# Kernel optimization log

Hardware: AMD Instinct MI355X
Metric: run time of the kernel (lower is better)

The kernel has to match this reference:

```python
import jax, jax.numpy as jnp
import numpy as np

B, N, C = 1, 6400, 256
NUM_CAMS, NUM_HEADS, NUM_LEVELS, NUM_POINTS = 6, 8, 3, 8
LVL_SHAPES = [(64, 176), (32, 88), (16, 44)]
IMG_H, IMG_W = 512, 1408


def setup_inputs():
    key = jax.random.key(0)
    ks = jax.random.split(key, 16)
    # Gaussian means in ego frame: depth z in [2,40]; x/y scaled so projections land in-image
    z = jax.random.uniform(ks[0], (B, N, 1), minval=2.0, maxval=40.0)
    xy = jax.random.uniform(ks[1], (B, N, 2), minval=-0.5, maxval=0.5)
    means = jnp.concatenate([xy[..., 0:1] * z * 0.8, xy[..., 1:2] * z * 0.4, z], -1)
    feature = jax.random.normal(ks[2], (B, N, C)) * 0.5
    feat0 = jax.random.normal(ks[3], (B * NUM_CAMS, C, 64, 176)) * 0.5
    feat1 = jax.random.normal(ks[4], (B * NUM_CAMS, C, 32, 88)) * 0.5
    feat2 = jax.random.normal(ks[5], (B * NUM_CAMS, C, 16, 44)) * 0.5
    cam2ego = jnp.tile(jnp.eye(4), (B, NUM_CAMS, 1, 1))
    cam2ego = cam2ego.at[..., :3, 3].set(jax.random.uniform(ks[6], (B, NUM_CAMS, 3), minval=-0.5, maxval=0.5))
    intrins = jnp.tile(jnp.array([[500., 0., 704.], [0., 500., 256.], [0., 0., 1.]]), (B, NUM_CAMS, 1, 1))
    post_rots = jnp.tile(jnp.eye(3), (B, NUM_CAMS, 1, 1))
    post_trans = jnp.concatenate([jax.random.uniform(ks[7], (B, NUM_CAMS, 2), minval=-30., maxval=30.),
                                  jnp.zeros((B, NUM_CAMS, 1))], -1)
    # deformable-attn style bias init for sampling offsets (as in init_weights)
    thetas = np.arange(NUM_HEADS) * (2.0 * np.pi / NUM_HEADS)
    grid = np.stack([np.cos(thetas), np.sin(thetas)], -1)
    grid = grid / np.abs(grid).max(-1, keepdims=True)
    grid = np.tile(grid.reshape(NUM_HEADS, 1, 1, 2), (1, NUM_LEVELS, NUM_POINTS, 1))
    grid = grid * (np.arange(NUM_POINTS) + 1).reshape(1, 1, NUM_POINTS, 1)
    b_off = jnp.asarray(grid.reshape(-1), jnp.float32)
    W_off = jax.random.normal(ks[8], (C, NUM_HEADS * NUM_LEVELS * NUM_POINTS * 2)) * 0.01
    W_attn = jax.random.normal(ks[9], (C, NUM_HEADS * NUM_LEVELS * NUM_POINTS)) * 0.02
    b_attn = jnp.zeros((NUM_HEADS * NUM_LEVELS * NUM_POINTS,))
    W_val = jax.random.normal(ks[10], (C, C)) * (1.0 / np.sqrt(C))
    b_val = jnp.zeros((C,))
    W_out = jax.random.normal(ks[11], (C, C)) * (1.0 / np.sqrt(C))
    b_out = jnp.zeros((C,))
    cams_embeds = jax.random.normal(ks[12], (NUM_CAMS, C))
    level_embeds = jax.random.normal(ks[13], (NUM_LEVELS, C))
    ln_g = jnp.ones((C,))
    ln_b = jnp.zeros((C,))
    return dict(means=means, feature=feature, feat0=feat0, feat1=feat1, feat2=feat2,
                cam2ego=cam2ego, intrins=intrins, post_rots=post_rots, post_trans=post_trans,
                W_off=W_off, b_off=b_off, W_attn=W_attn, b_attn=b_attn, W_val=W_val, b_val=b_val,
                W_out=W_out, b_out=b_out, cams_embeds=cams_embeds, level_embeds=level_embeds,
                ln_g=ln_g, ln_b=ln_b, img_h=IMG_H, img_w=IMG_W)


def _msda(value, shapes, loc, attn):
    # Multi-scale deformable attention (matches multi_scale_deformable_attn_pytorch,
    # i.e. grid_sample bilinear, align_corners=False, zero padding).
    # value [Bc,S,H,D]; loc [Bc,Nq,H,L,P,2] in [0,1]; attn [Bc,Nq,H,L,P]
    Bc, S, Hh, D = value.shape
    Nq, P = loc.shape[1], loc.shape[4]
    out = jnp.zeros((Bc, Hh, Nq, D), value.dtype)
    start = 0
    for lvl, (h, w) in enumerate(shapes):
        v = value[:, start:start + h * w].transpose(0, 2, 1, 3)  # [Bc,H,h*w,D]
        l = loc[:, :, :, lvl]                                    # [Bc,Nq,H,P,2]
        x = l[..., 0] * w - 0.5  # align_corners=False pixel coords
        y = l[..., 1] * h - 0.5
        x0 = jnp.floor(x)
        y0 = jnp.floor(y)
        tx = x - x0
        ty = y - y0
        a = attn[:, :, :, lvl]                                   # [Bc,Nq,H,P]
        def samp(xi, yi, wgt):
            valid = (xi >= 0) & (xi <= w - 1) & (yi >= 0) & (yi <= h - 1)
            idx = (jnp.clip(yi, 0, h - 1) * w + jnp.clip(xi, 0, w - 1)).astype(jnp.int32)
            idx = idx.transpose(0, 2, 1, 3).reshape(Bc, Hh, Nq * P)
            g = jnp.take_along_axis(v, idx[..., None], axis=2)   # [Bc,H,Nq*P,D]
            coef = wgt * jnp.where(valid, 1.0, 0.0).astype(v.dtype) * a
            return g * coef.transpose(0, 2, 1, 3).reshape(Bc, Hh, Nq * P, 1)
        acc = (samp(x0, y0, (1 - tx) * (1 - ty)) + samp(x0 + 1, y0, tx * (1 - ty))
               + samp(x0, y0 + 1, (1 - tx) * ty) + samp(x0 + 1, y0 + 1, tx * ty))
        out = out + acc.reshape(Bc, Hh, Nq, P, D).sum(3)
        start += h * w
    return out.transpose(0, 2, 1, 3).reshape(Bc, Nq, Hh * D)


def reference(means, feature, feat0, feat1, feat2, cam2ego, intrins, post_rots, post_trans,
              W_off, b_off, W_attn, b_attn, W_val, b_val, W_out, b_out,
              cams_embeds, level_embeds, ln_g, ln_b, img_h, img_w):
    Bq, Nq, Cc = feature.shape
    D = Cc // NUM_HEADS
    # --- project reference points into each camera (project_reference_points) ---
    mh = jnp.concatenate([means, jnp.ones((Bq, Nq, 1), means.dtype)], -1)      # [B,N,4]
    means_cam = jnp.einsum('bcij,bnj->bcni', jnp.linalg.inv(cam2ego), mh)[..., :3]
    means_img = jnp.einsum('bcij,bcnj->bcni', intrins, means_cam)              # [B,cams,N,3]
    mi = jnp.concatenate([means_img[..., :2] / (means_img[..., 2:] + 1e-4), means_img[..., 2:]], -1)
    mi = jnp.einsum('bcij,bcnj->bcni', post_rots, mi) + post_trans[:, :, None, :]
    coor = mi[..., :2] / jnp.array([img_w, img_h], feature.dtype)              # [B,cams,N,2]
    depth = mi[..., 2]
    mask = ((depth > 0.01) & (coor[..., 0] > 0.) & (coor[..., 0] < 1.)
            & (coor[..., 1] > 0.) & (coor[..., 1] < 1.))                        # [B,cams,N]
    # --- per-query sampling offsets / attention weights (shared across cameras) ---
    offsets = (feature @ W_off + b_off).reshape(Bq, Nq, NUM_HEADS, NUM_LEVELS, NUM_POINTS, 2)
    attn = jax.nn.softmax((feature @ W_attn + b_attn).reshape(Bq, Nq, NUM_HEADS, NUM_LEVELS * NUM_POINTS), -1)
    attn = attn.reshape(Bq, Nq, NUM_HEADS, NUM_LEVELS, NUM_POINTS)
    # --- flatten multi-level feats + cam/level embeds, value projection ---
    feats = (feat0, feat1, feat2)
    shapes = [(f.shape[2], f.shape[3]) for f in feats]
    flat = []
    for lvl, f in enumerate(feats):
        h, w = shapes[lvl]
        fl = f.reshape(Bq, NUM_CAMS, Cc, h * w)
        fl = fl + cams_embeds[None, :, :, None] + level_embeds[lvl][None, None, :, None]
        flat.append(fl)
    value = jnp.concatenate(flat, -1).transpose(0, 1, 3, 2).reshape(Bq * NUM_CAMS, -1, Cc)
    value = (value @ W_val + b_val).reshape(Bq * NUM_CAMS, -1, NUM_HEADS, D)
    # --- sampling locations per camera ---
    norm = jnp.array([[w, h] for (h, w) in shapes], feature.dtype)             # [L,2] = (W_l,H_l)
    loc = coor[:, :, :, None, None, None, :] + offsets[:, None] / norm[None, None, None, None, :, None, :]
    loc = loc.reshape(Bq * NUM_CAMS, Nq, NUM_HEADS, NUM_LEVELS, NUM_POINTS, 2)
    attn_bc = jnp.broadcast_to(attn[:, None], (Bq, NUM_CAMS, Nq, NUM_HEADS, NUM_LEVELS, NUM_POINTS))
    attn_bc = attn_bc.reshape(Bq * NUM_CAMS, Nq, NUM_HEADS, NUM_LEVELS, NUM_POINTS)
    out = _msda(value, shapes, loc, attn_bc).reshape(Bq, NUM_CAMS, Nq, Cc)
    # --- mask-weighted combine over cameras (mathematically equals the rebatch/scatter) ---
    mf = mask.astype(feature.dtype)
    slots = (out * mf[..., None]).sum(1) / jnp.maximum(mf.sum(1), 1.0)[..., None]
    slots = slots @ W_out + b_out
    x = slots + feature  # dropout is identity at inference
    mu = jnp.mean(x, -1, keepdims=True)
    var = jnp.mean((x - mu) ** 2, -1, keepdims=True)
    return (x - mu) / jnp.sqrt(var + 1e-5) * ln_g + ln_b
```

## Files before the change

### kernel.cpp

```cpp
#include <hip/hip_runtime.h>
#include <hip/hip_bf16.h>

typedef __bf16 bf16;
typedef __attribute__((ext_vector_type(4))) float f32x4;
typedef __attribute__((ext_vector_type(8))) bf16 bf16x8;
typedef __attribute__((ext_vector_type(2))) bf16 bf16x2;

#define NCAMS 6
#define NQ 6400
#define CH 256
#define NH 8
#define NL 3
#define NP 8
#define S_TOT 14784

#if __has_builtin(__builtin_amdgcn_fdot2_f32_bf16) && __has_builtin(__builtin_amdgcn_perm)
#define MSDA_DOT2 1
#else
#define MSDA_DOT2 0
#endif

__global__ __launch_bounds__(256) void k_prep(
    const float* __restrict__ means, const float* __restrict__ cam2ego,
    const float* __restrict__ intrins, const float* __restrict__ post_rots,
    const float* __restrict__ post_trans, const int* __restrict__ img_h,
    const int* __restrict__ img_w,
    const float* __restrict__ W_val, const float* __restrict__ W_off,
    const float* __restrict__ W_attn, const float* __restrict__ W_out,
    float* __restrict__ coor, float* __restrict__ maskf,
    bf16* __restrict__ Wvp, bf16* __restrict__ Woap, bf16* __restrict__ Wop)
{
    int bid = blockIdx.x;
    if (bid < 150) {
        int idx = bid * 256 + threadIdx.x;
        if (idx >= NCAMS * NQ) return;
        int cam = idx / NQ, n = idx % NQ;
        float mx = means[n*3+0], my = means[n*3+1], mz = means[n*3+2];
        const float* M = cam2ego + cam*16;
        float R[3][3], t[3];
        #pragma unroll
        for (int r = 0; r < 3; r++) {
            #pragma unroll
            for (int c = 0; c < 3; c++) R[r][c] = M[r*4+c];
            t[r] = M[r*4+3];
        }
        float dx = mx - t[0], dy = my - t[1], dz = mz - t[2];
        float xc = R[0][0]*dx + R[1][0]*dy + R[2][0]*dz;
        float yc = R[0][1]*dx + R[1][1]*dy + R[2][1]*dz;
        float zc = R[0][2]*dx + R[1][2]*dy + R[2][2]*dz;
        const float* K = intrins + cam*9;
        float ix = K[0]*xc + K[1]*yc + K[2]*zc;
        float iy = K[3]*xc + K[4]*yc + K[5]*zc;
        float iz = K[6]*xc + K[7]*yc + K[8]*zc;
        float px = ix / (iz + 1e-4f), py = iy / (iz + 1e-4f), pz = iz;
        const float* P = post_rots + cam*9;
        const float* T = post_trans + cam*3;
        float vx = P[0]*px + P[1]*py + P[2]*pz + T[0];
        float vy = P[3]*px + P[4]*py + P[5]*pz + T[1];
        float vz = P[6]*px + P[7]*py + P[8]*pz + T[2];
        float cx = vx / (float)img_w[0];
        float cy = vy / (float)img_h[0];
        bool ok = (vz > 0.01f) && (cx > 0.f) && (cx < 1.f) && (cy > 0.f) && (cy < 1.f);
        coor[idx*2+0] = cx;
        coor[idx*2+1] = cy;
        maskf[idx] = ok ? 1.f : 0.f;
        return;
    }
    int flat = (bid - 150) * 256 + threadIdx.x;
    if (flat < 8192) {
        int kc = flat >> 10, rem = flat & 1023;
        int nf = rem >> 6, lane = rem & 63;
        int q = lane >> 4, col = nf*16 + (lane & 15);
        bf16x8 v;
        #pragma unroll
        for (int j = 0; j < 8; j++) v[j] = (bf16)W_val[(size_t)(kc*32 + q*8 + j)*256 + col];
        *reinterpret_cast<bf16x8*>(Wvp + (size_t)flat*8) = v;
    } else if (flat < 26624) {
        int f2 = flat - 8192;
        int kc = f2 / (36*64), rem = f2 % (36*64);
        int nf = rem >> 6, lane = rem & 63;
        int q = lane >> 4, col = nf*16 + (lane & 15);
        bf16x8 v;
        #pragma unroll
        for (int j = 0; j < 8; j++) {
            int k = kc*32 + q*8 + j;
            float x = (col < 384) ? W_off[(size_t)k*384 + col] : W_attn[(size_t)k*192 + (col-384)];
            v[j] = (bf16)x;
        }
        *reinterpret_cast<bf16x8*>(Woap + (size_t)f2*8) = v;
    } else if (flat < 34816) {
        int f3 = flat - 26624;
        int kc = f3 >> 10, rem = f3 & 1023;
        int nf = rem >> 6, lane = rem & 63;
        int q = lane >> 4, col = nf*16 + (lane & 15);
        bf16x8 v;
        #pragma unroll
        for (int j = 0; j < 8; j++) v[j] = (bf16)W_out[(size_t)(kc*32 + q*8 + j)*256 + col];
        *reinterpret_cast<bf16x8*>(Wop + (size_t)f3*8) = v;
    }
}

__global__ __launch_bounds__(256) void k_offattn2(
    const float* __restrict__ feature, const bf16* __restrict__ Woap,
    const float* __restrict__ b_off, const float* __restrict__ b_attn,
    float* __restrict__ offs, bf16* __restrict__ attn_out)
{
    __shared__ float lg[16][200];
    int t = threadIdx.x, lane = t & 63, w = t >> 6;
    int q = lane >> 4, r16 = lane & 15;
    int n0 = blockIdx.x * 16;

    f32x4 acc[9];
    #pragma unroll
    for (int i = 0; i < 9; i++) acc[i] = (f32x4){0.f,0.f,0.f,0.f};

    const float* arow = feature + (size_t)(n0 + r16)*CH;
    for (int kc = 0; kc < 8; kc++) {
        f32x4 a0 = *reinterpret_cast<const f32x4*>(arow + kc*32 + q*8);
        f32x4 a1 = *reinterpret_cast<const f32x4*>(arow + kc*32 + q*8 + 4);
        bf16x8 afr;
        #pragma unroll
        for (int i = 0; i < 4; i++) { afr[i] = (bf16)a0[i]; afr[4+i] = (bf16)a1[i]; }
        #pragma unroll
        for (int nf9 = 0; nf9 < 9; nf9++) {
            bf16x8 bfr = *reinterpret_cast<const bf16x8*>(Woap + ((size_t)(kc*36 + w*9 + nf9)*64 + lane)*8);
            acc[nf9] = __builtin_amdgcn_mfma_f32_16x16x32_bf16(afr, bfr, acc[nf9], 0, 0, 0);
        }
    }
    #pragma unroll
    for (int nf9 = 0; nf9 < 9; nf9++) {
        int nfg = w*9 + nf9;
        int nglob = nfg*16 + r16;
        if (nfg < 24) {
            float bias = b_off[nglob];
            #pragma unroll
            for (int r = 0; r < 4; r++)
                offs[(size_t)(n0 + q*4 + r)*384 + nglob] = acc[nf9][r] + bias;
        } else {
            int la = nglob - 384;
            float bias = b_attn[la];
            #pragma unroll
            for (int r = 0; r < 4; r++)
                lg[q*4 + r][la] = acc[nf9][r] + bias;
        }
    }
    __syncthreads();
    if (t < 128) {
        int m = t >> 3, h = t & 7;
        const float* L = &lg[m][h*24];
        float mx = -1e30f;
        #pragma unroll
        for (int j = 0; j < 24; j++) mx = fmaxf(mx, L[j]);
        float e[24]; float s = 0.f;
        #pragma unroll
        for (int j = 0; j < 24; j++) { e[j] = __expf(L[j] - mx); s += e[j]; }
        float inv = 1.f / s;
        #pragma unroll
        for (int j = 0; j < 24; j++) attn_out[(size_t)(n0+m)*192 + h*24 + j] = (bf16)(e[j]*inv);
    }
}

__global__ __launch_bounds__(256) void k_valproj(
    const float* __restrict__ f0, const float* __restrict__ f1, const float* __restrict__ f2,
    const float* __restrict__ cams_embeds, const float* __restrict__ level_embeds,
    const bf16* __restrict__ Wvp, const float* __restrict__ b_val, bf16* __restrict__ value)
{
    __shared__ alignas(16) bf16 A[64][48];
    __shared__ alignas(16) bf16 Cst[16][256];
    int bi = blockIdx.x;
    int cam = bi / 231, mb = bi % 231;
    int lvl, local0, HW;
    const float* fp;
    if (mb < 176)      { lvl = 0; local0 = mb*64;        fp = f0; HW = 11264; }
    else if (mb < 220) { lvl = 1; local0 = (mb-176)*64;  fp = f1; HW = 2816;  }
    else               { lvl = 2; local0 = (mb-220)*64;  fp = f2; HW = 704;   }
    int pos0 = (lvl == 0 ? 0 : (lvl == 1 ? 11264 : 14080)) + local0;
    const float* featbase = fp + (size_t)cam*CH*HW + local0;

    int t = threadIdx.x;
    int lane = t & 63, w = t >> 6;
    int kk = t >> 3;
    int m8 = (t & 7) * 8;
    int q = lane >> 4, r16 = lane & 15;

    f32x4 acc[4][4];
    #pragma unroll
    for (int i = 0; i < 4; i++)
        #pragma unroll
        for (int j = 0; j < 4; j++) acc[i][j] = (f32x4){0.f,0.f,0.f,0.f};

    for (int kc = 0; kc < 8; kc++) {
        __syncthreads();
        int kg = kc*32 + kk;
        float e = cams_embeds[cam*CH + kg] + level_embeds[lvl*CH + kg];
        f32x4 v0 = *reinterpret_cast<const f32x4*>(featbase + (size_t)kg*HW + m8);
        f32x4 v1 = *reinterpret_cast<const f32x4*>(featbase + (size_t)kg*HW + m8 + 4);
        #pragma unroll
        for (int i = 0; i < 4; i++) A[m8+i][kk]   = (bf16)(v0[i] + e);
        #pragma unroll
        for (int i = 0; i < 4; i++) A[m8+4+i][kk] = (bf16)(v1[i] + e);
        __syncthreads();

        bf16x8 bfr[4];
        #pragma unroll
        for (int nf = 0; nf < 4; nf++) {
            int nfg = w*4 + nf;
            bfr[nf] = *reinterpret_cast<const bf16x8*>(Wvp + ((size_t)(kc*16 + nfg)*64 + lane)*8);
        }
        #pragma unroll
        for (int mf = 0; mf < 4; mf++) {
            bf16x8 afr = *reinterpret_cast<const bf16x8*>(&A[mf*16 + r16][q*8]);
            #pragma unroll
            for (int nf = 0; nf < 4; nf++)
                acc[mf][nf] = __builtin_amdgcn_mfma_f32_16x16x32_bf16(afr, bfr[nf], acc[mf][nf], 0, 0, 0);
        }
    }
    int orow = t >> 4;
    int ocol = (t & 15) * 16;
    int ohead = ocol >> 5, och = ocol & 31;
    #pragma unroll
    for (int mf = 0; mf < 4; mf++) {
        __syncthreads();
        #pragma unroll
        for (int nf = 0; nf < 4; nf++) {
            int c = w*64 + nf*16 + r16;
            float bv = b_val[c];
            #pragma unroll
            for (int r = 0; r < 4; r++)
                Cst[q*4 + r][c] = (bf16)(acc[mf][nf][r] + bv);
        }
        __syncthreads();
        int srow = pos0 + mf*16 + orow;
        bf16* dst = value + ((size_t)(cam*NH + ohead)*S_TOT + srow)*32 + och;
        const f32x4* src = reinterpret_cast<const f32x4*>(&Cst[orow][ocol]);
        f32x4 x0 = src[0], x1 = src[1];
        reinterpret_cast<f32x4*>(dst)[0] = x0;
        reinterpret_cast<f32x4*>(dst)[1] = x1;
    }
}

__global__ __launch_bounds__(256) void k_msda(
    const float* __restrict__ coor, const float* __restrict__ offs,
    const bf16* __restrict__ attn, const bf16* __restrict__ value,
    const float* __restrict__ maskf, float* __restrict__ slots)
{
    __shared__ int4  s_o[NCAMS*192];
#if MSDA_DOT2
    __shared__ uint2 s_w[NCAMS*192];
#else
    __shared__ f32x4 s_w[NCAMS*192];
#endif
    int n = blockIdx.x;
    int t = threadIdx.x;

    for (int it = t; it < NCAMS*192; it += 256) {
        int cam = it / 192;
        int r   = it - cam*192;
        int hh  = r / 24;
        int rr  = r - hh*24;
        int lvl = rr >> 3;

        float mk = maskf[cam*NQ + n];
        float cx = coor[(cam*NQ + n)*2 + 0];
        float cy = coor[(cam*NQ + n)*2 + 1];
        float2 o2 = *reinterpret_cast<const float2*>(offs + (size_t)n*384 + r*2);
        float aw = (float)attn[(size_t)n*192 + r] * mk;

        int wi   = (lvl == 0) ? 176 : ((lvl == 1) ? 88 : 44);
        int hi   = (lvl == 0) ? 64  : ((lvl == 1) ? 32 : 16);
        int base = (lvl == 0) ? 0   : ((lvl == 1) ? 11264 : 14080);

        float x = cx*(float)wi + o2.x - 0.5f;
        float y = cy*(float)hi + o2.y - 0.5f;
        float xf = floorf(x), yf = floorf(y);
        float tx = x - xf, ty = y - yf;
        float wm1x = (float)(wi-1), wm1y = (float)(hi-1);
        bool vx0 = (xf >= 0.f)      && (xf <= wm1x);
        bool vx1 = (xf+1.f >= 0.f)  && (xf+1.f <= wm1x);
        bool vy0 = (yf >= 0.f)      && (yf <= wm1y);
        bool vy1 = (yf+1.f >= 0.f)  && (yf+1.f <= wm1y);
        int x0 = (int)fminf(fmaxf(xf,      0.f), wm1x);
        int x1 = (int)fminf(fmaxf(xf+1.f,  0.f), wm1x);
        int y0 = (int)fminf(fmaxf(yf,      0.f), wm1y);
        int y1 = (int)fminf(fmaxf(yf+1.f,  0.f), wm1y);
        float w00 = (1.f-tx)*(1.f-ty)*aw * ((vx0 && vy0) ? 1.f : 0.f);
        float w10 = tx*(1.f-ty)*aw       * ((vx1 && vy0) ? 1.f : 0.f);
        float w01 = (1.f-tx)*ty*aw       * ((vx0 && vy1) ? 1.f : 0.f);
        float w11 = tx*ty*aw             * ((vx1 && vy1) ? 1.f : 0.f);
        int rowb = (cam*NH + hh)*S_TOT + base;
        int r0 = rowb + y0*wi, r1 = rowb + y1*wi;
        s_o[it] = make_int4((r0 + x0)*64, (r0 + x1)*64, (r1 + x0)*64, (r1 + x1)*64);
#if MSDA_DOT2
        bf16x2 wa; wa[0] = (bf16)w00; wa[1] = (bf16)w10;
        bf16x2 wb; wb[0] = (bf16)w01; wb[1] = (bf16)w11;
        s_w[it] = make_uint2(__builtin_bit_cast(unsigned, wa),
                             __builtin_bit_cast(unsigned, wb));
#else
        s_w[it] = (f32x4){w00, w10, w01, w11};
#endif
    }
    __syncthreads();

    int lane = t & 63, wv = t >> 6;
    int hl = lane >> 5;
    int p  = (lane >> 2) & 7;
    int k2 = lane & 3;
    int hglob = wv*2 + hl;
    int kb = k2 * 16;
    int ibase = hglob*24 + p;

    f32x4 acc0 = (f32x4){0.f,0.f,0.f,0.f};
    f32x4 acc1 = (f32x4){0.f,0.f,0.f,0.f};
    const char* vbyte = (const char*)value;

    #pragma unroll 2
    for (int cam = 0; cam < NCAMS; cam++) {
        #pragma unroll
        for (int lvl = 0; lvl < 3; lvl++) {
            int it = cam*192 + ibase + lvl*8;
            int4  o4 = s_o[it];
#if MSDA_DOT2
            uint2 wp = s_w[it];
            bf16x2 wa = __builtin_bit_cast(bf16x2, wp.x);
            bf16x2 wb = __builtin_bit_cast(bf16x2, wp.y);
            uint4 d00 = *reinterpret_cast<const uint4*>(vbyte + (o4.x + kb));
            uint4 d10 = *reinterpret_cast<const uint4*>(vbyte + (o4.y + kb));
            uint4 d01 = *reinterpret_cast<const uint4*>(vbyte + (o4.z + kb));
            uint4 d11 = *reinterpret_cast<const uint4*>(vbyte + (o4.w + kb));
            unsigned a0 = __builtin_amdgcn_perm(d10.x, d00.x, 0x05040100u);
            unsigned a1 = __builtin_amdgcn_perm(d10.x, d00.x, 0x07060302u);
            unsigned a2 = __builtin_amdgcn_perm(d10.y, d00.y, 0x05040100u);
            unsigned a3 = __builtin_amdgcn_perm(d10.y, d00.y, 0x07060302u);
            unsigned a4 = __builtin_amdgcn_perm(d10.z, d00.z, 0x05040100u);
            unsigned a5 = __builtin_amdgcn_perm(d10.z, d00.z, 0x07060302u);
            unsigned a6 = __builtin_amdgcn_perm(d10.w, d00.w, 0x05040100u);
            unsigned a7 = __builtin_amdgcn_perm(d10.w, d00.w, 0x07060302u);
            acc0[0] = __builtin_amdgcn_fdot2_f32_bf16(__builtin_bit_cast(bf16x2, a0), wa, acc0[0], false);
            acc0[1] = __builtin_amdgcn_fdot2_f32_bf16(__builtin_bit_cast(bf16x2, a1), wa, acc0[1], false);
            acc0[2] = __builtin_amdgcn_fdot2_f32_bf16(__builtin_bit_cast(bf16x2, a2), wa, acc0[2], false);
            acc0[3] = __builtin_amdgcn_fdot2_f32_bf16(__builtin_bit_cast(bf16x2, a3), wa, acc0[3], false);
            acc1[0] = __builtin_amdgcn_fdot2_f32_bf16(__builtin_bit_cast(bf16x2, a4), wa, acc1[0], false);
            acc1[1] = __builtin_amdgcn_fdot2_f32_bf16(__builtin_bit_cast(bf16x2, a5), wa, acc1[1], false);
            acc1[2] = __builtin_amdgcn_fdot2_f32_bf16(__builtin_bit_cast(bf16x2, a6), wa, acc1[2], false);
            acc1[3] = __builtin_amdgcn_fdot2_f32_bf16(__builtin_bit_cast(bf16x2, a7), wa, acc1[3], false);
            unsigned b0 = __builtin_amdgcn_perm(d11.x, d01.x, 0x05040100u);
            unsigned b1 = __builtin_amdgcn_perm(d11.x, d01.x, 0x07060302u);
            unsigned b2 = __builtin_amdgcn_perm(d11.y, d01.y, 0x05040100u);
            unsigned b3 = __builtin_amdgcn_perm(d11.y, d01.y, 0x07060302u);
            unsigned b4 = __builtin_amdgcn_perm(d11.z, d01.z, 0x05040100u);
            unsigned b5 = __builtin_amdgcn_perm(d11.z, d01.z, 0x07060302u);
            unsigned b6 = __builtin_amdgcn_perm(d11.w, d01.w, 0x05040100u);
            unsigned b7 = __builtin_amdgcn_perm(d11.w, d01.w, 0x07060302u);
            acc0[0] = __builtin_amdgcn_fdot2_f32_bf16(__builtin_bit_cast(bf16x2, b0), wb, acc0[0], false);
            acc0[1] = __builtin_amdgcn_fdot2_f32_bf16(__builtin_bit_cast(bf16x2, b1), wb, acc0[1], false);
            acc0[2] = __builtin_amdgcn_fdot2_f32_bf16(__builtin_bit_cast(bf16x2, b2), wb, acc0[2], false);
            acc0[3] = __builtin_amdgcn_fdot2_f32_bf16(__builtin_bit_cast(bf16x2, b3), wb, acc0[3], false);
            acc1[0] = __builtin_amdgcn_fdot2_f32_bf16(__builtin_bit_cast(bf16x2, b4), wb, acc1[0], false);
            acc1[1] = __builtin_amdgcn_fdot2_f32_bf16(__builtin_bit_cast(bf16x2, b5), wb, acc1[1], false);
            acc1[2] = __builtin_amdgcn_fdot2_f32_bf16(__builtin_bit_cast(bf16x2, b6), wb, acc1[2], false);
            acc1[3] = __builtin_amdgcn_fdot2_f32_bf16(__builtin_bit_cast(bf16x2, b7), wb, acc1[3], false);
#else
            f32x4 w4 = s_w[it];
            uint4 d00 = *reinterpret_cast<const uint4*>(vbyte + (o4.x + kb));
            uint4 d10 = *reinterpret_cast<const uint4*>(vbyte + (o4.y + kb));
            uint4 d01 = *reinterpret_cast<const uint4*>(vbyte + (o4.z + kb));
            uint4 d11 = *reinterpret_cast<const uint4*>(vbyte + (o4.w + kb));
            acc0[0] = fmaf(__uint_as_float(d00.x << 16),         w4.x, acc0[0]);
            acc0[1] = fmaf(__uint_as_float(d00.x & 0xffff0000u), w4.x, acc0[1]);
            acc0[2] = fmaf(__uint_as_float(d00.y << 16),         w4.x, acc0[2]);
            acc0[3] = fmaf(__uint_as_float(d00.y & 0xffff0000u), w4.x, acc0[3]);
            acc1[0] = fmaf(__uint_as_float(d00.z << 16),         w4.x, acc1[0]);
            acc1[1] = fmaf(__uint_as_float(d00.z & 0xffff0000u), w4.x, acc1[1]);
            acc1[2] = fmaf(__uint_as_float(d00.w << 16),         w4.x, acc1[2]);
            acc1[3] = fmaf(__uint_as_float(d00.w & 0xffff0000u), w4.x, acc1[3]);
            acc0[0] = fmaf(__uint_as_float(d10.x << 16),         w4.y, acc0[0]);
            acc0[1] = fmaf(__uint_as_float(d10.x & 0xffff0000u), w4.y, acc0[1]);
            acc0[2] = fmaf(__uint_as_float(d10.y << 16),         w4.y, acc0[2]);
            acc0[3] = fmaf(__uint_as_float(d10.y & 0xffff0000u), w4.y, acc0[3]);
            acc1[0] = fmaf(__uint_as_float(d10.z << 16),         w4.y, acc1[0]);
            acc1[1] = fmaf(__uint_as_float(d10.z & 0xffff0000u), w4.y, acc1[1]);
            acc1[2] = fmaf(__uint_as_float(d10.w << 16),         w4.y, acc1[2]);
            acc1[3] = fmaf(__uint_as_float(d10.w & 0xffff0000u), w4.y, acc1[3]);
            acc0[0] = fmaf(__uint_as_float(d01.x << 16),         w4.z, acc0[0]);
            acc0[1] = fmaf(__uint_as_float(d01.x & 0xffff0000u), w4.z, acc0[1]);
            acc0[2] = fmaf(__uint_as_float(d01.y << 16),         w4.z, acc0[2]);
            acc0[3] = fmaf(__uint_as_float(d01.y & 0xffff0000u), w4.z, acc0[3]);
            acc1[0] = fmaf(__uint_as_float(d01.z << 16),         w4.z, acc1[0]);
            acc1[1] = fmaf(__uint_as_float(d01.z & 0xffff0000u), w4.z, acc1[1]);
            acc1[2] = fmaf(__uint_as_float(d01.w << 16),         w4.z, acc1[2]);
            acc1[3] = fmaf(__uint_as_float(d01.w & 0xffff0000u), w4.z, acc1[3]);
            acc0[0] = fmaf(__uint_as_float(d11.x << 16),         w4.w, acc0[0]);
            acc0[1] = fmaf(__uint_as_float(d11.x & 0xffff0000u), w4.w, acc0[1]);
            acc0[2] = fmaf(__uint_as_float(d11.y << 16),         w4.w, acc0[2]);
            acc0[3] = fmaf(__uint_as_float(d11.y & 0xffff0000u), w4.w, acc0[3]);
            acc1[0] = fmaf(__uint_as_float(d11.z << 16),         w4.w, acc1[0]);
            acc1[1] = fmaf(__uint_as_float(d11.z & 0xffff0000u), w4.w, acc1[1]);
            acc1[2] = fmaf(__uint_as_float(d11.w << 16),         w4.w, acc1[2]);
            acc1[3] = fmaf(__uint_as_float(d11.w & 0xffff0000u), w4.w, acc1[3]);
#endif
        }
    }

    #pragma unroll
    for (int i = 0; i < 4; i++) {
        acc0[i] += __shfl_xor(acc0[i], 4);
        acc0[i] += __shfl_xor(acc0[i], 8);
        acc0[i] += __shfl_xor(acc0[i], 16);
        acc1[i] += __shfl_xor(acc1[i], 4);
        acc1[i] += __shfl_xor(acc1[i], 8);
        acc1[i] += __shfl_xor(acc1[i], 16);
    }
    if (p == 0) {
        float* dst = slots + (size_t)n*CH + hglob*32 + k2*8;
        *reinterpret_cast<f32x4*>(dst)     = acc0;
        *reinterpret_cast<f32x4*>(dst + 4) = acc1;
    }
}

__global__ __launch_bounds__(256) void k_final2(
    const float* __restrict__ slots, const float* __restrict__ maskf,
    const bf16* __restrict__ Wop, const float* __restrict__ b_out,
    const float* __restrict__ feature, const float* __restrict__ ln_g,
    const float* __restrict__ ln_b, float* __restrict__ out)
{
    __shared__ float yb[16][264];
    int t = threadIdx.x, lane = t & 63, w = t >> 6;
    int q = lane >> 4, r16 = lane & 15;
    int n0 = blockIdx.x * 16;

    float msum = 0.f;
    #pragma unroll
    for (int cam = 0; cam < NCAMS; cam++) msum += maskf[cam*NQ + n0 + r16];
    float inv = 1.f / fmaxf(msum, 1.f);

    f32x4 acc[4];
    #pragma unroll
    for (int i = 0; i < 4; i++) acc[i] = (f32x4){0.f,0.f,0.f,0.f};

    const float* srow = slots + (size_t)(n0 + r16)*CH;
    for (int kc = 0; kc < 8; kc++) {
        f32x4 a0 = *reinterpret_cast<const f32x4*>(srow + kc*32 + q*8);
        f32x4 a1 = *reinterpret_cast<const f32x4*>(srow + kc*32 + q*8 + 4);
        bf16x8 afr;
        #pragma unroll
        for (int i = 0; i < 4; i++) { afr[i] = (bf16)(a0[i]*inv); afr[4+i] = (bf16)(a1[i]*inv); }
        #pragma unroll
        for (int nf = 0; nf < 4; nf++) {
            bf16x8 bfr = *reinterpret_cast<const bf16x8*>(Wop + ((size_t)(kc*16 + w*4 + nf)*64 + lane)*8);
            acc[nf] = __builtin_amdgcn_mfma_f32_16x16x32_bf16(afr, bfr, acc[nf], 0, 0, 0);
        }
    }
    #pragma unroll
    for (int nf = 0; nf < 4; nf++) {
        int c = (w*4 + nf)*16 + r16;
        float bias = b_out[c];
        #pragma unroll
        for (int r = 0; r < 4; r++) {
            int m = q*4 + r;
            yb[m][c] = acc[nf][r] + bias + feature[(size_t)(n0+m)*CH + c];
        }
    }
    __syncthreads();
    int row = t >> 4, l16 = t & 15;
    int c0 = l16 * 16;
    float s = 0.f, s2 = 0.f;
    #pragma unroll
    for (int j = 0; j < 16; j++) {
        float v = yb[row][c0 + j];
        s += v; s2 += v*v;
    }
    #pragma unroll
    for (int off = 1; off < 16; off <<= 1) {
        s  += __shfl_xor(s, off);
        s2 += __shfl_xor(s2, off);
    }
    float mu = s / 256.f;
    float rsig = rsqrtf(s2 / 256.f - mu*mu + 1e-5f);
    float* orow = out + (size_t)(n0 + row)*CH + c0;
    #pragma unroll
    for (int j4 = 0; j4 < 4; j4++) {
        f32x4 o;
        #pragma unroll
        for (int i = 0; i < 4; i++) {
            int c = c0 + j4*4 + i;
            o[i] = (yb[row][c] - mu) * rsig * ln_g[c] + ln_b[c];
        }
        *reinterpret_cast<f32x4*>(orow + j4*4) = o;
    }
}

extern "C" void kernel_launch(void* const* d_in, const int* in_sizes, int n_in,
                              void* d_out, int out_size, void* d_ws, size_t ws_size,
                              hipStream_t stream)
{
    const float* means       = (const float*)d_in[0];
    const float* feature     = (const float*)d_in[1];
    const float* feat0       = (const float*)d_in[2];
    const float* feat1       = (const float*)d_in[3];
    const float* feat2       = (const float*)d_in[4];
    const float* cam2ego     = (const float*)d_in[5];
    const float* intrins     = (const float*)d_in[6];
    const float* post_rots   = (const float*)d_in[7];
    const float* post_trans  = (const float*)d_in[8];
    const float* W_off       = (const float*)d_in[9];
    const float* b_off       = (const float*)d_in[10];
    const float* W_attn      = (const float*)d_in[11];
    const float* b_attn      = (const float*)d_in[12];
    const float* W_val       = (const float*)d_in[13];
    const float* b_val       = (const float*)d_in[14];
    const float* W_out       = (const float*)d_in[15];
    const float* b_out       = (const float*)d_in[16];
    const float* cams_embeds = (const float*)d_in[17];
    const float* level_embeds= (const float*)d_in[18];
    const float* ln_g        = (const float*)d_in[19];
    const float* ln_b        = (const float*)d_in[20];
    const int*   img_h       = (const int*)d_in[21];
    const int*   img_w       = (const int*)d_in[22];

    char* ws = (char*)d_ws;
    float* coor  = (float*)(ws + 0);
    float* maskf = (float*)(ws + 307200);
    float* offs  = (float*)(ws + 460800);
    bf16*  attn  = (bf16*) (ws + 10291200);
    bf16*  Wvp   = (bf16*) (ws + 12748800);
    bf16*  Woap  = (bf16*) (ws + 12879872);
    bf16*  Wop   = (bf16*) (ws + 13174784);
    float* slots = (float*)(ws + 13305856);
    bf16*  value = (bf16*) (ws + 19859456);
    if (ws_size < 65275904u) return;

    k_prep    <<<286, 256, 0, stream>>>(means, cam2ego, intrins, post_rots, post_trans,
                                        img_h, img_w, W_val, W_off, W_attn, W_out,
                                        coor, maskf, Wvp, Woap, Wop);
    k_offattn2<<<400, 256, 0, stream>>>(feature, Woap, b_off, b_attn, offs, attn);
    k_valproj <<<1386, 256, 0, stream>>>(feat0, feat1, feat2, cams_embeds, level_embeds, Wvp, b_val, value);
    k_msda    <<<6400, 256, 0, stream>>>(coor, offs, attn, value, maskf, slots);
    k_final2  <<<400, 256, 0, stream>>>(slots, maskf, Wop, b_out, feature, ln_g, ln_b, (float*)d_out);
}
```

Before: 302.8 us.

## Merge offset/attn and value-projection kernels; software-pipeline MSDA gathers across cameras

Folds the offset/attention projection and the value projection into one launch, branching on block index, so both independent GEMMs share a single grid and one launch and drain. In the MSDA sampling loop, the 12 value gathers for the next camera are issued before the current camera's bilinear dot products are computed, hiding gather latency. The trade-offs are higher register pressure, which may lower occupancy, and shared memory sized for the larger of the two merged paths.

```diff
diff --git a/kernel.cpp b/kernel.cpp
--- a/kernel.cpp
+++ b/kernel.cpp
@@ -100,74 +100,76 @@
     }
 }
 
-__global__ __launch_bounds__(256) void k_offattn2(
+__global__ __launch_bounds__(256) void k_mid(
     const float* __restrict__ feature, const bf16* __restrict__ Woap,
     const float* __restrict__ b_off, const float* __restrict__ b_attn,
-    float* __restrict__ offs, bf16* __restrict__ attn_out)
-{
-    __shared__ float lg[16][200];
-    int t = threadIdx.x, lane = t & 63, w = t >> 6;
-    int q = lane >> 4, r16 = lane & 15;
-    int n0 = blockIdx.x * 16;
-
-    f32x4 acc[9];
-    #pragma unroll
-    for (int i = 0; i < 9; i++) acc[i] = (f32x4){0.f,0.f,0.f,0.f};
-
-    const float* arow = feature + (size_t)(n0 + r16)*CH;
-    for (int kc = 0; kc < 8; kc++) {
-        f32x4 a0 = *reinterpret_cast<const f32x4*>(arow + kc*32 + q*8);
-        f32x4 a1 = *reinterpret_cast<const f32x4*>(arow + kc*32 + q*8 + 4);
-        bf16x8 afr;
-        #pragma unroll
-        for (int i = 0; i < 4; i++) { afr[i] = (bf16)a0[i]; afr[4+i] = (bf16)a1[i]; }
-        #pragma unroll
-        for (int nf9 = 0; nf9 < 9; nf9++) {
-            bf16x8 bfr = *reinterpret_cast<const bf16x8*>(Woap + ((size_t)(kc*36 + w*9 + nf9)*64 + lane)*8);
-            acc[nf9] = __builtin_amdgcn_mfma_f32_16x16x32_bf16(afr, bfr, acc[nf9], 0, 0, 0);
-        }
-    }
-    #pragma unroll
-    for (int nf9 = 0; nf9 < 9; nf9++) {
-        int nfg = w*9 + nf9;
-        int nglob = nfg*16 + r16;
-        if (nfg < 24) {
-            float bias = b_off[nglob];
-            #pragma unroll
-            for (int r = 0; r < 4; r++)
-                offs[(size_t)(n0 + q*4 + r)*384 + nglob] = acc[nf9][r] + bias;
-        } else {
-            int la = nglob - 384;
-            float bias = b_attn[la];
-            #pragma unroll
-            for (int r = 0; r < 4; r++)
-                lg[q*4 + r][la] = acc[nf9][r] + bias;
-        }
-    }
-    __syncthreads();
-    if (t < 128) {
-        int m = t >> 3, h = t & 7;
-        const float* L = &lg[m][h*24];
-        float mx = -1e30f;
-        #pragma unroll
-        for (int j = 0; j < 24; j++) mx = fmaxf(mx, L[j]);
-        float e[24]; float s = 0.f;
-        #pragma unroll
-        for (int j = 0; j < 24; j++) { e[j] = __expf(L[j] - mx); s += e[j]; }
-        float inv = 1.f / s;
-        #pragma unroll
-        for (int j = 0; j < 24; j++) attn_out[(size_t)(n0+m)*192 + h*24 + j] = (bf16)(e[j]*inv);
-    }
-}
-
-__global__ __launch_bounds__(256) void k_valproj(
+    float* __restrict__ offs, bf16* __restrict__ attn_out,
     const float* __restrict__ f0, const float* __restrict__ f1, const float* __restrict__ f2,
     const float* __restrict__ cams_embeds, const float* __restrict__ level_embeds,
     const bf16* __restrict__ Wvp, const float* __restrict__ b_val, bf16* __restrict__ value)
 {
-    __shared__ alignas(16) bf16 A[64][48];
-    __shared__ alignas(16) bf16 Cst[16][256];
-    int bi = blockIdx.x;
+    __shared__ alignas(16) char smem[14336];
+    int t = threadIdx.x, lane = t & 63, w = t >> 6;
+    int q = lane >> 4, r16 = lane & 15;
+
+    if (blockIdx.x < 400) {
+        float (*lg)[200] = reinterpret_cast<float(*)[200]>(smem);
+        int n0 = blockIdx.x * 16;
+
+        f32x4 acc[9];
+        #pragma unroll
+        for (int i = 0; i < 9; i++) acc[i] = (f32x4){0.f,0.f,0.f,0.f};
+
+        const float* arow = feature + (size_t)(n0 + r16)*CH;
+        for (int kc = 0; kc < 8; kc++) {
+            f32x4 a0 = *reinterpret_cast<const f32x4*>(arow + kc*32 + q*8);
+            f32x4 a1 = *reinterpret_cast<const f32x4*>(arow + kc*32 + q*8 + 4);
+            bf16x8 afr;
+            #pragma unroll
+            for (int i = 0; i < 4; i++) { afr[i] = (bf16)a0[i]; afr[4+i] = (bf16)a1[i]; }
+            #pragma unroll
+            for (int nf9 = 0; nf9 < 9; nf9++) {
+                bf16x8 bfr = *reinterpret_cast<const bf16x8*>(Woap + ((size_t)(kc*36 + w*9 + nf9)*64 + lane)*8);
+                acc[nf9] = __builtin_amdgcn_mfma_f32_16x16x32_bf16(afr, bfr, acc[nf9], 0, 0, 0);
+            }
+        }
+        #pragma unroll
+        for (int nf9 = 0; nf9 < 9; nf9++) {
+            int nfg = w*9 + nf9;
+            int nglob = nfg*16 + r16;
+            if (nfg < 24) {
+                float bias = b_off[nglob];
+                #pragma unroll
+                for (int r = 0; r < 4; r++)
+                    offs[(size_t)(n0 + q*4 + r)*384 + nglob] = acc[nf9][r] + bias;
+            } else {
+                int la = nglob - 384;
+                float bias = b_attn[la];
+                #pragma unroll
+                for (int r = 0; r < 4; r++)
+                    lg[q*4 + r][la] = acc[nf9][r] + bias;
+            }
+        }
+        __syncthreads();
+        if (t < 128) {
+            int m = t >> 3, h = t & 7;
+            const float* L = &lg[m][h*24];
+            float mx = -1e30f;
+            #pragma unroll
+            for (int j = 0; j < 24; j++) mx = fmaxf(mx, L[j]);
+            float e[24]; float s = 0.f;
+            #pragma unroll
+            for (int j = 0; j < 24; j++) { e[j] = __expf(L[j] - mx); s += e[j]; }
+            float inv = 1.f / s;
+            #pragma unroll
+            for (int j = 0; j < 24; j++) attn_out[(size_t)(n0+m)*192 + h*24 + j] = (bf16)(e[j]*inv);
+        }
+        return;
+    }
+
+    bf16 (*A)[48]    = reinterpret_cast<bf16(*)[48]>(smem);
+    bf16 (*Cst)[256] = reinterpret_cast<bf16(*)[256]>(smem + 6144);
+    int bi = blockIdx.x - 400;
     int cam = bi / 231, mb = bi % 231;
     int lvl, local0, HW;
     const float* fp;
@@ -177,11 +179,8 @@
     int pos0 = (lvl == 0 ? 0 : (lvl == 1 ? 11264 : 14080)) + local0;
     const float* featbase = fp + (size_t)cam*CH*HW + local0;
 
-    int t = threadIdx.x;
-    int lane = t & 63, w = t >> 6;
     int kk = t >> 3;
     int m8 = (t & 7) * 8;
-    int q = lane >> 4, r16 = lane & 15;
 
     f32x4 acc[4][4];
     #pragma unroll
@@ -313,93 +312,127 @@
     f32x4 acc1 = (f32x4){0.f,0.f,0.f,0.f};
     const char* vbyte = (const char*)value;
 
-    #pragma unroll 2
+    uint4 cA0,cA1,cA2, cB0,cB1,cB2, cC0,cC1,cC2, cD0,cD1,cD2;
+#if MSDA_DOT2
+    uint2 cw0, cw1, cw2;
+#else
+    f32x4 cw0, cw1, cw2;
+#endif
+
+#define LOADBATCH(CAMIDX, A0,A1,A2, B0,B1,B2, C0,C1,C2, D0,D1,D2, W0,W1,W2) \
+    { int itb = (CAMIDX)*192 + ibase; \
+      int4 o0 = s_o[itb]; int4 o1 = s_o[itb+8]; int4 o2v = s_o[itb+16]; \
+      A0 = *reinterpret_cast<const uint4*>(vbyte + (o0.x + kb)); \
+      B0 = *reinterpret_cast<const uint4*>(vbyte + (o0.y + kb)); \
+      C0 = *reinterpret_cast<const uint4*>(vbyte + (o0.z + kb)); \
+      D0 = *reinterpret_cast<const uint4*>(vbyte + (o0.w + kb)); \
+      A1 = *reinterpret_cast<const uint4*>(vbyte + (o1.x + kb)); \
+      B1 = *reinterpret_cast<const uint4*>(vbyte + (o1.y + kb)); \
+      C1 = *reinterpret_cast<const uint4*>(vbyte + (o1.z + kb)); \
+      D1 = *reinterpret_cast<const uint4*>(vbyte + (o1.w + kb)); \
+      A2 = *reinterpret_cast<const uint4*>(vbyte + (o2v.x + kb)); \
+      B2 = *reinterpret_cast<const uint4*>(vbyte + (o2v.y + kb)); \
+      C2 = *reinterpret_cast<const uint4*>(vbyte + (o2v.z + kb)); \
+      D2 = *reinterpret_cast<const uint4*>(vbyte + (o2v.w + kb)); \
+      W0 = s_w[itb]; W1 = s_w[itb+8]; W2 = s_w[itb+16]; }
+
+#if MSDA_DOT2
+#define CONSUME1(d00, d10, d01, d11, WP) \
+    { bf16x2 wa = __builtin_bit_cast(bf16x2, (WP).x); \
+      bf16x2 wb = __builtin_bit_cast(bf16x2, (WP).y); \
+      unsigned a0 = __builtin_amdgcn_perm((d10).x, (d00).x, 0x05040100u); \
+      unsigned a1 = __builtin_amdgcn_perm((d10).x, (d00).x, 0x07060302u); \
+      unsigned a2 = __builtin_amdgcn_perm((d10).y, (d00).y, 0x05040100u); \
+      unsigned a3 = __builtin_amdgcn_perm((d10).y, (d00).y, 0x07060302u); \
+      unsigned a4 = __builtin_amdgcn_perm((d10).z, (d00).z, 0x05040100u); \
+      unsigned a5 = __builtin_amdgcn_perm((d10).z, (d00).z, 0x07060302u); \
+      unsigned a6 = __builtin_amdgcn_perm((d10).w, (d00).w, 0x05040100u); \
+      unsigned a7 = __builtin_amdgcn_perm((d10).w, (d00).w, 0x07060302u); \
+      acc0[0] = __builtin_amdgcn_fdot2_f32_bf16(__builtin_bit_cast(bf16x2, a0), wa, acc0[0], false); \
+      acc0[1] = __builtin_amdgcn_fdot2_f32_bf16(__builtin_bit_cast(bf16x2, a1), wa, acc0[1], false); \
+      acc0[2] = __builtin_amdgcn_fdot2_f32_bf16(__builtin_bit_cast(bf16x2, a2), wa, acc0[2], false); \
+      acc0[3] = __builtin_amdgcn_fdot2_f32_bf16(__builtin_bit_cast(bf16x2, a3), wa, acc0[3], false); \
+      acc1[0] = __builtin_amdgcn_fdot2_f32_bf16(__builtin_bit_cast(bf16x2, a4), wa, acc1[0], false); \
+      acc1[1] = __builtin_amdgcn_fdot2_f32_bf16(__builtin_bit_cast(bf16x2, a5), wa, acc1[1], false); \
+      acc1[2] = __builtin_amdgcn_fdot2_f32_bf16(__builtin_bit_cast(bf16x2, a6), wa, acc1[2], false); \
+      acc1[3] = __builtin_amdgcn_fdot2_f32_bf16(__builtin_bit_cast(bf16x2, a7), wa, acc1[3], false); \
+      unsigned b0 = __builtin_amdgcn_perm((d11).x, (d01).x, 0x05040100u); \
+      unsigned b1 = __builtin_amdgcn_perm((d11).x, (d01).x, 0x07060302u); \
+      unsigned b2 = __builtin_amdgcn_perm((d11).y, (d01).y, 0x05040100u); \
+      unsigned b3 = __builtin_amdgcn_perm((d11).y, (d01).y, 0x07060302u); \
+      unsigned b4 = __builtin_amdgcn_perm((d11).z, (d01).z, 0x05040100u); \
+      unsigned b5 = __builtin_amdgcn_perm((d11).z, (d01).z, 0x07060302u); \
+      unsigned b6 = __builtin_amdgcn_perm((d11).w, (d01).w, 0x05040100u); \
+      unsigned b7 = __builtin_amdgcn_perm((d11).w, (d01).w, 0x07060302u); \
+      acc0[0] = __builtin_amdgcn_fdot2_f32_bf16(__builtin_bit_cast(bf16x2, b0), wb, acc0[0], false); \
+      acc0[1] = __builtin_amdgcn_fdot2_f32_bf16(__builtin_bit_cast(bf16x2, b1), wb, acc0[1], false); \
+      acc0[2] = __builtin_amdgcn_fdot2_f32_bf16(__builtin_bit_cast(bf16x2, b2), wb, acc0[2], false); \
+      acc0[3] = __builtin_amdgcn_fdot2_f32_bf16(__builtin_bit_cast(bf16x2, b3), wb, acc0[3], false); \
+      acc1[0] = __builtin_amdgcn_fdot2_f32_bf16(__builtin_bit_cast(bf16x2, b4), wb, acc1[0], false); \
+      acc1[1] = __builtin_amdgcn_fdot2_f32_bf16(__builtin_bit_cast(bf16x2, b5), wb, acc1[1], false); \
+      acc1[2] = __builtin_amdgcn_fdot2_f32_bf16(__builtin_bit_cast(bf16x2, b6), wb, acc1[2], false); \
+      acc1[3] = __builtin_amdgcn_fdot2_f32_bf16(__builtin_bit_cast(bf16x2, b7), wb, acc1[3], false); }
+#else
+#define CONSUME1(d00, d10, d01, d11, WP) \
+    { f32x4 w4 = (WP); \
+      acc0[0] = fmaf(__uint_as_float((d00).x << 16),         w4.x, acc0[0]); \
+      acc0[1] = fmaf(__uint_as_float((d00).x & 0xffff0000u), w4.x, acc0[1]); \
+      acc0[2] = fmaf(__uint_as_float((d00).y << 16),         w4.x, acc0[2]); \
+      acc0[3] = fmaf(__uint_as_float((d00).y & 0xffff0000u), w4.x, acc0[3]); \
+      acc1[0] = fmaf(__uint_as_float((d00).z << 16),         w4.x, acc1[0]); \
+      acc1[1] = fmaf(__uint_as_float((d00).z & 0xffff0000u), w4.x, acc1[1]); \
+      acc1[2] = fmaf(__uint_as_float((d00).w << 16),         w4.x, acc1[2]); \
+      acc1[3] = fmaf(__uint_as_float((d00).w & 0xffff0000u), w4.x, acc1[3]); \
+      acc0[0] = fmaf(__uint_as_float((d10).x << 16),         w4.y, acc0[0]); \
+      acc0[1] = fmaf(__uint_as_float((d10).x & 0xffff0000u), w4.y, acc0[1]); \
+      acc0[2] = fmaf(__uint_as_float((d10).y << 16),         w4.y, acc0[2]); \
+      acc0[3] = fmaf(__uint_as_float((d10).y & 0xffff0000u), w4.y, acc0[3]); \
+      acc1[0] = fmaf(__uint_as_float((d10).z << 16),         w4.y, acc1[0]); \
+      acc1[1] = fmaf(__uint_as_float((d10).z & 0xffff0000u), w4.y, acc1[1]); \
+      acc1[2] = fmaf(__uint_as_float((d10).w << 16),         w4.y, acc1[2]); \
+      acc1[3] = fmaf(__uint_as_float((d10).w & 0xffff0000u), w4.y, acc1[3]); \
+      acc0[0] = fmaf(__uint_as_float((d01).x << 16),         w4.z, acc0[0]); \
+      acc0[1] = fmaf(__uint_as_float((d01).x & 0xffff0000u), w4.z, acc0[1]); \
+      acc0[2] = fmaf(__uint_as_float((d01).y << 16),         w4.z, acc0[2]); \
+      acc0[3] = fmaf(__uint_as_float((d01).y & 0xffff0000u), w4.z, acc0[3]); \
+      acc1[0] = fmaf(__uint_as_float((d01).z << 16),         w4.z, acc1[0]); \
+      acc1[1] = fmaf(__uint_as_float((d01).z & 0xffff0000u), w4.z, acc1[1]); \
+      acc1[2] = fmaf(__uint_as_float((d01).w << 16),         w4.z, acc1[2]); \
+      acc1[3] = fmaf(__uint_as_float((d01).w & 0xffff0000u), w4.z, acc1[3]); \
+      acc0[0] = fmaf(__uint_as_float((d11).x << 16),         w4.w, acc0[0]); \
+      acc0[1] = fmaf(__uint_as_float((d11).x & 0xffff0000u), w4.w, acc0[1]); \
+      acc0[2] = fmaf(__uint_as_float((d11).y << 16),         w4.w, acc0[2]); \
+      acc0[3] = fmaf(__uint_as_float((d11).y & 0xffff0000u), w4.w, acc0[3]); \
+      acc1[0] = fmaf(__uint_as_float((d11).z << 16),         w4.w, acc1[0]); \
+      acc1[1] = fmaf(__uint_as_float((d11).z & 0xffff0000u), w4.w, acc1[1]); \
+      acc1[2] = fmaf(__uint_as_float((d11).w << 16),         w4.w, acc1[2]); \
+      acc1[3] = fmaf(__uint_as_float((d11).w & 0xffff0000u), w4.w, acc1[3]); }
+#endif
+
+    LOADBATCH(0, cA0,cA1,cA2, cB0,cB1,cB2, cC0,cC1,cC2, cD0,cD1,cD2, cw0,cw1,cw2)
+
+    #pragma unroll
     for (int cam = 0; cam < NCAMS; cam++) {
-        #pragma unroll
-        for (int lvl = 0; lvl < 3; lvl++) {
-            int it = cam*192 + ibase + lvl*8;
-            int4  o4 = s_o[it];
+        uint4 nA0,nA1,nA2, nB0,nB1,nB2, nC0,nC1,nC2, nD0,nD1,nD2;
 #if MSDA_DOT2
-            uint2 wp = s_w[it];
-            bf16x2 wa = __builtin_bit_cast(bf16x2, wp.x);
-            bf16x2 wb = __builtin_bit_cast(bf16x2, wp.y);
-            uint4 d00 = *reinterpret_cast<const uint4*>(vbyte + (o4.x + kb));
-            uint4 d10 = *reinterpret_cast<const uint4*>(vbyte + (o4.y + kb));
-            uint4 d01 = *reinterpret_cast<const uint4*>(vbyte + (o4.z + kb));
-            uint4 d11 = *reinterpret_cast<const uint4*>(vbyte + (o4.w + kb));
-            unsigned a0 = __builtin_amdgcn_perm(d10.x, d00.x, 0x05040100u);
-            unsigned a1 = __builtin_amdgcn_perm(d10.x, d00.x, 0x07060302u);
-            unsigned a2 = __builtin_amdgcn_perm(d10.y, d00.y, 0x05040100u);
-            unsigned a3 = __builtin_amdgcn_perm(d10.y, d00.y, 0x07060302u);
-            unsigned a4 = __builtin_amdgcn_perm(d10.z, d00.z, 0x05040100u);
-            unsigned a5 = __builtin_amdgcn_perm(d10.z, d00.z, 0x07060302u);
-            unsigned a6 = __builtin_amdgcn_perm(d10.w, d00.w, 0x05040100u);
-            unsigned a7 = __builtin_amdgcn_perm(d10.w, d00.w, 0x07060302u);
-            acc0[0] = __builtin_amdgcn_fdot2_f32_bf16(__builtin_bit_cast(bf16x2, a0), wa, acc0[0], false);
-            acc0[1] = __builtin_amdgcn_fdot2_f32_bf16(__builtin_bit_cast(bf16x2, a1), wa, acc0[1], false);
-            acc0[2] = __builtin_amdgcn_fdot2_f32_bf16(__builtin_bit_cast(bf16x2, a2), wa, acc0[2], false);
-            acc0[3] = __builtin_amdgcn_fdot2_f32_bf16(__builtin_bit_cast(bf16x2, a3), wa, acc0[3], false);
-            acc1[0] = __builtin_amdgcn_fdot2_f32_bf16(__builtin_bit_cast(bf16x2, a4), wa, acc1[0], false);
-            acc1[1] = __builtin_amdgcn_fdot2_f32_bf16(__builtin_bit_cast(bf16x2, a5), wa, acc1[1], false);
-            acc1[2] = __builtin_amdgcn_fdot2_f32_bf16(__builtin_bit_cast(bf16x2, a6), wa, acc1[2], false);
-            acc1[3] = __builtin_amdgcn_fdot2_f32_bf16(__builtin_bit_cast(bf16x2, a7), wa, acc1[3], false);
-            unsigned b0 = __builtin_amdgcn_perm(d11.x, d01.x, 0x05040100u);
-            unsigned b1 = __builtin_amdgcn_perm(d11.x, d01.x, 0x07060302u);
-            unsigned b2 = __builtin_amdgcn_perm(d11.y, d01.y, 0x05040100u);
-            unsigned b3 = __builtin_amdgcn_perm(d11.y, d01.y, 0x07060302u);
-            unsigned b4 = __builtin_amdgcn_perm(d11.z, d01.z, 0x05040100u);
-            unsigned b5 = __builtin_amdgcn_perm(d11.z, d01.z, 0x07060302u);
-            unsigned b6 = __builtin_amdgcn_perm(d11.w, d01.w, 0x05040100u);
-            unsigned b7 = __builtin_amdgcn_perm(d11.w, d01.w, 0x07060302u);
-            acc0[0] = __builtin_amdgcn_fdot2_f32_bf16(__builtin_bit_cast(bf16x2, b0), wb, acc0[0], false);
-            acc0[1] = __builtin_amdgcn_fdot2_f32_bf16(__builtin_bit_cast(bf16x2, b1), wb, acc0[1], false);
-            acc0[2] = __builtin_amdgcn_fdot2_f32_bf16(__builtin_bit_cast(bf16x2, b2), wb, acc0[2], false);
-            acc0[3] = __builtin_amdgcn_fdot2_f32_bf16(__builtin_bit_cast(bf16x2, b3), wb, acc0[3], false);
-            acc1[0] = __builtin_amdgcn_fdot2_f32_bf16(__builtin_bit_cast(bf16x2, b4), wb, acc1[0], false);
-            acc1[1] = __builtin_amdgcn_fdot2_f32_bf16(__builtin_bit_cast(bf16x2, b5), wb, acc1[1], false);
-            acc1[2] = __builtin_amdgcn_fdot2_f32_bf16(__builtin_bit_cast(bf16x2, b6), wb, acc1[2], false);
-            acc1[3] = __builtin_amdgcn_fdot2_f32_bf16(__builtin_bit_cast(bf16x2, b7), wb, acc1[3], false);
+        uint2 nw0, nw1, nw2;
 #else
-            f32x4 w4 = s_w[it];
-            uint4 d00 = *reinterpret_cast<const uint4*>(vbyte + (o4.x + kb));
-            uint4 d10 = *reinterpret_cast<const uint4*>(vbyte + (o4.y + kb));
-            uint4 d01 = *reinterpret_cast<const uint4*>(vbyte + (o4.z + kb));
-            uint4 d11 = *reinterpret_cast<const uint4*>(vbyte + (o4.w + kb));
-            acc0[0] = fmaf(__uint_as_float(d00.x << 16),         w4.x, acc0[0]);
-            acc0[1] = fmaf(__uint_as_float(d00.x & 0xffff0000u), w4.x, acc0[1]);
-            acc0[2] = fmaf(__uint_as_float(d00.y << 16),         w4.x, acc0[2]);
-            acc0[3] = fmaf(__uint_as_float(d00.y & 0xffff0000u), w4.x, acc0[3]);
-            acc1[0] = fmaf(__uint_as_float(d00.z << 16),         w4.x, acc1[0]);
-            acc1[1] = fmaf(__uint_as_float(d00.z & 0xffff0000u), w4.x, acc1[1]);
-            acc1[2] = fmaf(__uint_as_float(d00.w << 16),         w4.x, acc1[2]);
-            acc1[3] = fmaf(__uint_as_float(d00.w & 0xffff0000u), w4.x, acc1[3]);
-            acc0[0] = fmaf(__uint_as_float(d10.x << 16),         w4.y, acc0[0]);
-            acc0[1] = fmaf(__uint_as_float(d10.x & 0xffff0000u), w4.y, acc0[1]);
-            acc0[2] = fmaf(__uint_as_float(d10.y << 16),         w4.y, acc0[2]);
-            acc0[3] = fmaf(__uint_as_float(d10.y & 0xffff0000u), w4.y, acc0[3]);
-            acc1[0] = fmaf(__uint_as_float(d10.z << 16),         w4.y, acc1[0]);
-            acc1[1] = fmaf(__uint_as_float(d10.z & 0xffff0000u), w4.y, acc1[1]);
-            acc1[2] = fmaf(__uint_as_float(d10.w << 16),         w4.y, acc1[2]);
-            acc1[3] = fmaf(__uint_as_float(d10.w & 0xffff0000u), w4.y, acc1[3]);
-            acc0[0] = fmaf(__uint_as_float(d01.x << 16),         w4.z, acc0[0]);
-            acc0[1] = fmaf(__uint_as_float(d01.x & 0xffff0000u), w4.z, acc0[1]);
-            acc0[2] = fmaf(__uint_as_float(d01.y << 16),         w4.z, acc0[2]);
-            acc0[3] = fmaf(__uint_as_float(d01.y & 0xffff0000u), w4.z, acc0[3]);
-            acc1[0] = fmaf(__uint_as_float(d01.z << 16),         w4.z, acc1[0]);
-            acc1[1] = fmaf(__uint_as_float(d01.z & 0xffff0000u), w4.z, acc1[1]);
-            acc1[2] = fmaf(__uint_as_float(d01.w << 16),         w4.z, acc1[2]);
-            acc1[3] = fmaf(__uint_as_float(d01.w & 0xffff0000u), w4.z, acc1[3]);
-            acc0[0] = fmaf(__uint_as_float(d11.x << 16),         w4.w, acc0[0]);
-            acc0[1] = fmaf(__uint_as_float(d11.x & 0xffff0000u), w4.w, acc0[1]);
-            acc0[2] = fmaf(__uint_as_float(d11.y << 16),         w4.w, acc0[2]);
-            acc0[3] = fmaf(__uint_as_float(d11.y & 0xffff0000u), w4.w, acc0[3]);
-            acc1[0] = fmaf(__uint_as_float(d11.z << 16),         w4.w, acc1[0]);
-            acc1[1] = fmaf(__uint_as_float(d11.z & 0xffff0000u), w4.w, acc1[1]);
-            acc1[2] = fmaf(__uint_as_float(d11.w << 16),         w4.w, acc1[2]);
-            acc1[3] = fmaf(__uint_as_float(d11.w & 0xffff0000u), w4.w, acc1[3]);
+        f32x4 nw0, nw1, nw2;
 #endif
-        }
-    }
+        if (cam + 1 < NCAMS) {
+            LOADBATCH(cam+1, nA0,nA1,nA2, nB0,nB1,nB2, nC0,nC1,nC2, nD0,nD1,nD2, nw0,nw1,nw2)
+        }
+        CONSUME1(cA0, cB0, cC0, cD0, cw0)
+        CONSUME1(cA1, cB1, cC1, cD1, cw1)
+        CONSUME1(cA2, cB2, cC2, cD2, cw2)
+        if (cam + 1 < NCAMS) {
+            cA0=nA0; cA1=nA1; cA2=nA2; cB0=nB0; cB1=nB1; cB2=nB2;
+            cC0=nC0; cC1=nC1; cC2=nC2; cD0=nD0; cD1=nD1; cD2=nD2;
+            cw0=nw0; cw1=nw1; cw2=nw2;
+        }
+    }
+#undef LOADBATCH
+#undef CONSUME1
 
     #pragma unroll
     for (int i = 0; i < 4; i++) {
@@ -529,11 +562,12 @@
     bf16*  value = (bf16*) (ws + 19859456);
     if (ws_size < 65275904u) return;
 
-    k_prep    <<<286, 256, 0, stream>>>(means, cam2ego, intrins, post_rots, post_trans,
-                                        img_h, img_w, W_val, W_off, W_attn, W_out,
-                                        coor, maskf, Wvp, Woap, Wop);
-    k_offattn2<<<400, 256, 0, stream>>>(feature, Woap, b_off, b_attn, offs, attn);
-    k_valproj <<<1386, 256, 0, stream>>>(feat0, feat1, feat2, cams_embeds, level_embeds, Wvp, b_val, value);
-    k_msda    <<<6400, 256, 0, stream>>>(coor, offs, attn, value, maskf, slots);
-    k_final2  <<<400, 256, 0, stream>>>(slots, maskf, Wop, b_out, feature, ln_g, ln_b, (float*)d_out);
+    k_prep  <<<286, 256, 0, stream>>>(means, cam2ego, intrins, post_rots, post_trans,
+                                      img_h, img_w, W_val, W_off, W_attn, W_out,
+                                      coor, maskf, Wvp, Woap, Wop);
+    k_mid   <<<1786, 256, 0, stream>>>(feature, Woap, b_off, b_attn, offs, attn,
+                                       feat0, feat1, feat2, cams_embeds, level_embeds,
+                                       Wvp, b_val, value);
+    k_msda  <<<6400, 256, 0, stream>>>(coor, offs, attn, value, maskf, slots);
+    k_final2<<<400, 256, 0, stream>>>(slots, maskf, Wop, b_out, feature, ln_g, ln_b, (float*)d_out);
 }
```

Result: no change. 308.4 us (+1.8%).
